# Kernel tuning notes

Measured on AMD Instinct MI355X. Metric: run time of the kernel, lower is better.

The kernel has to match this reference:

```python
import jax, jax.numpy as jnp
import numpy as np

PRE_NMS_THRESH = 0.05
PRE_NMS_TOP_N = 1000
NMS_THRESH = 0.6
FPN_POST_NMS_TOP_N = 100
MIN_SIZE = 0.0
STRIDE = 8
NEG = -1e9  # padding score for invalid slots (avoids inf/nan in grads)


def setup_inputs() -> dict:
    key = jax.random.key(0)
    k1, k2, k3 = jax.random.split(key, 3)
    N, H, W = 16, 400, 608
    # stride-8 FCOS location grid, xy order
    xs = (jnp.arange(W, dtype=jnp.float32) * STRIDE) + STRIDE // 2
    ys = (jnp.arange(H, dtype=jnp.float32) * STRIDE) + STRIDE // 2
    gy, gx = jnp.meshgrid(ys, xs, indexing='ij')
    locations = jnp.stack([gx.reshape(-1), gy.reshape(-1)], axis=1)  # [H*W, 2]
    box_cls = jax.random.normal(k1, (N, 1, H, W), dtype=jnp.float32)
    box_regression = jax.random.uniform(k2, (N, 4, H, W), dtype=jnp.float32) * 64.0
    centerness = jax.random.normal(k3, (N, 1, H, W), dtype=jnp.float32)
    image_sizes = jnp.tile(jnp.array([[H * STRIDE, W * STRIDE]], dtype=jnp.int32), (N, 1))  # (h, w)
    return {"locations": locations, "box_cls": box_cls,
            "box_regression": box_regression, "centerness": centerness,
            "image_sizes": image_sizes}


def _nms_one(boxes, scores):
    """Greedy NMS over K fixed slots. boxes [K,4], scores [K] (NEG = invalid)."""
    order = jnp.argsort(-scores)
    b = boxes[order]
    s = scores[order]
    area = (b[:, 2] - b[:, 0]) * (b[:, 3] - b[:, 1])
    lt = jnp.maximum(b[:, None, :2], b[None, :, :2])   # [K,K,2]
    rb = jnp.minimum(b[:, None, 2:], b[None, :, 2:])
    wh = jnp.clip(rb - lt, 0.0)
    inter = wh[..., 0] * wh[..., 1]
    iou = inter / (area[:, None] + area[None, :] - inter + 1e-9)
    K = b.shape[0]
    ar = jnp.arange(K)

    def body(keep, i):
        kept_i = keep[i] & (s[i] > NEG / 2)
        keep = keep & ~(kept_i & (iou[i] > NMS_THRESH) & (ar > i))
        return keep, kept_i

    _, kept = jax.lax.scan(body, jnp.ones((K,), dtype=bool), ar)
    s_out = jnp.where(kept & (s > NEG / 2), s, NEG)
    return b, s_out


def reference(locations, box_cls, box_regression, centerness, image_sizes):
    N, C, H, W = box_cls.shape
    # [N,C,H,W] -> [N,H*W,C] ; BINARY, num_classes=2 -> C=1
    scores = jax.nn.sigmoid(box_cls.transpose(0, 2, 3, 1).reshape(N, -1))  # [N,HW]
    reg = box_regression.transpose(0, 2, 3, 1).reshape(N, -1, 4)           # [N,HW,4]
    ctr = jax.nn.sigmoid(centerness.transpose(0, 2, 3, 1).reshape(N, -1))  # [N,HW]
    cand = scores > PRE_NMS_THRESH           # candidate mask from raw cls score
    s = scores * ctr                         # score used for ranking
    sm = jnp.where(cand, s, NEG)
    vals, idx = jax.lax.top_k(sm, PRE_NMS_TOP_N)                 # [N,K]
    valid = jnp.take_along_axis(cand, idx, axis=1)               # [N,K]
    g_reg = jnp.take_along_axis(reg, idx[..., None], axis=1)     # [N,K,4]
    g_loc = locations[idx]                                       # [N,K,2]
    x1 = g_loc[..., 0] - g_reg[..., 0]
    y1 = g_loc[..., 1] - g_reg[..., 1]
    x2 = g_loc[..., 0] + g_reg[..., 2]
    y2 = g_loc[..., 1] + g_reg[..., 3]
    hw = image_sizes.astype(jnp.float32)
    wmax = hw[:, 1:2] - 1.0
    hmax = hw[:, 0:1] - 1.0
    x1 = jnp.clip(x1, 0.0, wmax); x2 = jnp.clip(x2, 0.0, wmax)
    y1 = jnp.clip(y1, 0.0, hmax); y2 = jnp.clip(y2, 0.0, hmax)
    keep_size = ((x2 - x1 + 1.0) >= MIN_SIZE) & ((y2 - y1 + 1.0) >= MIN_SIZE)
    valid = valid & keep_size
    boxes = jnp.stack([x1, y1, x2, y2], axis=-1)                 # [N,K,4]
    sc = jnp.where(valid, vals, NEG)
    b_sorted, s_nms = jax.vmap(_nms_one)(boxes, sc)              # [N,K,4],[N,K]
    fv, fi = jax.lax.top_k(s_nms, FPN_POST_NMS_TOP_N)            # [N,100]
    fb = jnp.take_along_axis(b_sorted, fi[..., None], axis=1)    # [N,100,4]
    fvalid = fv > NEG / 2
    fb = jnp.where(fvalid[..., None], fb, 0.0)
    fs = jnp.where(fvalid, fv, 0.0)
    labels = jnp.where(fvalid, 1, 0).astype(jnp.int32)
    dets = jnp.concatenate([fb, fs[..., None]], axis=-1)         # [N,100,5]
    return dets, labels, fvalid
```

## Files before the change

### kernel.cpp

```cpp
#include <hip/hip_runtime.h>
#include <cstdint>


#define NIMG 16
#define WW 608
#define HW 243200
#define NF4 60800
#define TOPK 1000
#define NBINS 512
#define NB2 2048
#define SCAN_BLOCKS 60
#define SCAN_THREADS 256
#define F4_PER_BLOCK 1024
#define LS 128
#define PCAP 1024
#define MCAP 2048
#define EDS_CAP 512
#define NEGV (-1e9f)

__device__ __forceinline__ float sigm(float x) { return 1.0f / (1.0f + expf(-x)); }

__device__ __forceinline__ int binof(float v) {
  if (!(v > 0.0f)) return 0;
  int b = (int)(v * (float)NBINS);
  return b > (NBINS - 1) ? (NBINS - 1) : b;
}

__device__ __forceinline__ int bucketof(float v) {
  if (!(v > 0.0f)) return 0;
  int b = (int)(v * (float)NB2);
  return b > (NB2 - 1) ? (NB2 - 1) : b;
}

__device__ __forceinline__ void find_thresh_bin(const unsigned* h, const unsigned* chunk,
                                                unsigned T, unsigned* outbs, int tid) {
  unsigned v = (tid < 32) ? chunk[tid] : 0u;
  unsigned inc = v;
#pragma unroll
  for (int d = 1; d < 32; d <<= 1) {
    unsigned o = __shfl_down(inc, d, 64);
    if (tid + d < 32) inc += o;
  }
  unsigned long long m = __ballot((tid < 32) && (inc >= T));
  if (m == 0ull) { if (tid == 0) *outbs = 0u; return; }
  int cc = 63 - __clzll(m);
  unsigned above = __shfl(inc, cc) - chunk[cc];
  unsigned v2 = (tid < 16) ? h[cc * 16 + tid] : 0u;
  unsigned inc2 = v2;
#pragma unroll
  for (int d = 1; d < 16; d <<= 1) {
    unsigned o = __shfl_down(inc2, d, 64);
    if (tid + d < 16) inc2 += o;
  }
  unsigned long long m2 = __ballot((tid < 16) && (above + inc2 >= T));
  int bb = (m2 != 0ull) ? (63 - __clzll(m2)) : 0;
  if (tid == 0) *outbs = (unsigned)(cc * 16 + bb);
}

__global__ __launch_bounds__(SCAN_THREADS) void k_scanstore(
    const float4* __restrict__ cls, const float4* __restrict__ ctr,
    unsigned long long* __restrict__ pre, unsigned* __restrict__ pcnt) {
  __shared__ unsigned lh[NBINS];
  __shared__ unsigned long long plist[PCAP];
  __shared__ unsigned chunk[NBINS / 16];
  __shared__ unsigned sLb, pcl;
  const int tid = threadIdx.x;
  for (int b = tid; b < NBINS; b += SCAN_THREADS) lh[b] = 0u;
  if (tid == 0) pcl = 0u;
  __syncthreads();
  const int n = blockIdx.y;
  const float4* c4 = cls + (size_t)n * NF4;
  const float4* t4 = ctr + (size_t)n * NF4;
  const int base = blockIdx.x * F4_PER_BLOCK;
  float4 cv[4], tv[4];
  float smr[16];
  bool ok[4];
#pragma unroll
  for (int e = 0; e < 4; ++e) {
    int i = base + e * SCAN_THREADS + tid;
    ok[e] = (i < NF4);
    if (ok[e]) { cv[e] = c4[i]; tv[e] = t4[i]; }
  }
#pragma unroll
  for (int e = 0; e < 4; ++e) {
    const float* cc = (const float*)&cv[e];
    const float* tt = (const float*)&tv[e];
#pragma unroll
    for (int k = 0; k < 4; ++k) {
      float sm = NEGV;
      if (ok[e]) {
        float sc = sigm(cc[k]);
        sm = (sc > 0.05f) ? sc * sigm(tt[k]) : NEGV;
        atomicAdd(&lh[binof(sm)], 1u);
      }
      smr[e * 4 + k] = sm;
    }
  }
  __syncthreads();
  if (tid < NBINS / 16) {
    unsigned s = 0;
    for (int k = 0; k < 16; ++k) s += lh[tid * 16 + k];
    chunk[tid] = s;
  }
  __syncthreads();
  if (tid < 64) find_thresh_bin(lh, chunk, LS, &sLb, tid);
  __syncthreads();
  const unsigned Lb = sLb;
#pragma unroll
  for (int e = 0; e < 4; ++e) {
    if (ok[e]) {
#pragma unroll
      for (int k = 0; k < 4; ++k) {
        float sm = smr[e * 4 + k];
        if ((unsigned)binof(sm) >= Lb) {
          unsigned gi = (unsigned)((base + e * SCAN_THREADS + tid) * 4 + k);
          unsigned p = atomicAdd(&pcl, 1u);
          if (p < PCAP)
            plist[p] = ((unsigned long long)__float_as_uint(sm) << 32) |
                       (unsigned long long)(~gi);
        }
      }
    }
  }
  __syncthreads();
  const int bslot = n * SCAN_BLOCKS + blockIdx.x;
  unsigned m = pcl; if (m > PCAP) m = PCAP;
  unsigned long long* gp = pre + (size_t)bslot * PCAP;
  for (unsigned k = tid; k < m; k += SCAN_THREADS) gp[k] = plist[k];
  if (tid == 0) pcnt[bslot] = m;
}

__global__ __launch_bounds__(1024) void k_fcr_nms(
    const unsigned long long* __restrict__ pre, const unsigned* __restrict__ pcnt,
    const float* __restrict__ reg, const int* __restrict__ isz,
    float* __restrict__ out) {
  __shared__ __align__(16) unsigned long long smemA[2816];
  __shared__ __align__(16) unsigned long long smemB[MCAP];
  __shared__ unsigned bh[NB2];
  __shared__ unsigned bbase[NB2];
  __shared__ unsigned chunk[32];
  __shared__ unsigned offs[SCAN_BLOCKS + 1];
  __shared__ unsigned wsum[16];
  __shared__ unsigned sB2, mc, ecl;
  const int n = blockIdx.x;
  const int tid = threadIdx.x;
  const int wid = tid >> 6, lane = tid & 63;
  unsigned long long* sk = smemB;

  for (int b = tid; b < NB2; b += 1024) bh[b] = 0u;
  if (tid < 64) {
    int l = tid;
    int v = (l < SCAN_BLOCKS) ? (int)pcnt[n * SCAN_BLOCKS + l] : 0;
    int inc = v;
#pragma unroll
    for (int d = 1; d < 64; d <<= 1) {
      int o = __shfl_up(inc, d, 64);
      if (l >= d) inc += o;
    }
    if (l < SCAN_BLOCKS) offs[l + 1] = (unsigned)inc;
    if (l == 0) offs[0] = 0u;
  }
  __syncthreads();
  const unsigned P = offs[SCAN_BLOCKS];
  const unsigned long long* pbase = pre + (size_t)n * SCAN_BLOCKS * PCAP;
  for (unsigned p = tid; p < P; p += 1024) {
    int lo = 0, hi = SCAN_BLOCKS - 1;
    while (lo < hi) {
      int mid = (lo + hi + 1) >> 1;
      if (offs[mid] <= p) lo = mid; else hi = mid - 1;
    }
    unsigned long long key = pbase[(size_t)lo * PCAP + (p - offs[lo])];
    float v = __uint_as_float((unsigned)(key >> 32));
    atomicAdd(&bh[bucketof(v)], 1u);
  }
  __syncthreads();
  if (tid < 32) {
    unsigned s = 0;
    const int b0 = tid * 64;
    for (int k = 0; k < 64; ++k) s += bh[b0 + k];
    chunk[tid] = s;
  }
  __syncthreads();
  if (tid < 64) {
    unsigned v = (tid < 32) ? chunk[tid] : 0u;
    unsigned inc = v;
#pragma unroll
    for (int d = 1; d < 32; d <<= 1) {
      unsigned o = __shfl_down(inc, d, 64);
      if (tid + d < 32) inc += o;
    }
    unsigned long long m = __ballot((tid < 32) && (inc >= TOPK));
    int cc = (m != 0ull) ? (63 - __clzll(m)) : 0;
    unsigned above = (m != 0ull) ? (__shfl(inc, cc) - chunk[cc]) : 0u;
    unsigned inc2 = bh[cc * 64 + tid];
#pragma unroll
    for (int d = 1; d < 64; d <<= 1) {
      unsigned o = __shfl_down(inc2, d, 64);
      if (tid + d < 64) inc2 += o;
    }
    unsigned long long m2 = __ballot(above + inc2 >= TOPK);
    int bb = (m2 != 0ull) ? (63 - __clzll(m2)) : 0;
    if (tid == 0) sB2 = (m != 0ull) ? (unsigned)(cc * 64 + bb) : 0u;
  }
  __syncthreads();
  const unsigned B2 = sB2;
  {
    int g0 = tid * 2, g1 = g0 + 1;
    unsigned a0 = bh[NB2 - 1 - g0];
    unsigned a1 = bh[NB2 - 1 - g1];
    unsigned pair = a0 + a1;
    unsigned inc = pair;
#pragma unroll
    for (int d = 1; d < 64; d <<= 1) {
      unsigned o = __shfl_up(inc, d, 64);
      if (lane >= d) inc += o;
    }
    if (lane == 63) wsum[wid] = inc;
    __syncthreads();
    if (tid < 64) {
      unsigned v = (tid < 16) ? wsum[tid] : 0u;
      unsigned i2 = v;
#pragma unroll
      for (int d = 1; d < 16; d <<= 1) {
        unsigned o = __shfl_up(i2, d, 64);
        if (tid >= d) i2 += o;
      }
      if (tid < 16) wsum[tid] = i2 - v;
    }
    __syncthreads();
    unsigned excl = inc - pair + wsum[wid];
    bbase[NB2 - 1 - g0] = excl;
    bbase[NB2 - 1 - g1] = excl + a0;
  }
  __syncthreads();
  if (tid == 0) {
    unsigned mm = bbase[B2] + bh[B2];
    mc = (mm > MCAP) ? MCAP : mm;
  }
  for (int b = tid; b < NB2; b += 1024) bh[b] = 0u;
  __syncthreads();
  const unsigned M = mc;
  for (unsigned p = tid; p < P; p += 1024) {
    int lo = 0, hi = SCAN_BLOCKS - 1;
    while (lo < hi) {
      int mid = (lo + hi + 1) >> 1;
      if (offs[mid] <= p) lo = mid; else hi = mid - 1;
    }
    unsigned long long key = pbase[(size_t)lo * PCAP + (p - offs[lo])];
    float v = __uint_as_float((unsigned)(key >> 32));
    int b = bucketof(v);
    if ((unsigned)b >= B2) {
      unsigned pos = bbase[b] + atomicAdd(&bh[b], 1u);
      if (pos < MCAP) sk[pos] = key;
    }
  }
  float4* sb = (float4*)smemA;
  float* ssc = (float*)((char*)smemA + 16384);
  unsigned char* kept = (unsigned char*)((char*)smemA + 20480);
  int* sel = (int*)((char*)smemA + 21600);
  if (tid < TOPK) { sb[tid] = make_float4(0.f, 0.f, 0.f, 0.f); ssc[tid] = NEGV; }
  __syncthreads();
  const float wmax = (float)(isz[n * 2 + 1] - 1);
  const float hmax = (float)(isz[n * 2 + 0] - 1);
  const float* rg = reg + (size_t)n * 4 * HW;
  for (unsigned s = tid; s < M; s += 1024) {
    const unsigned long long mykey = sk[s];
    int b = bucketof(__uint_as_float((unsigned)(mykey >> 32)));
    unsigned beg = bbase[b];
    unsigned end = (b > 0) ? bbase[b - 1] : M;
    if (end > M) end = M;
    unsigned rank = beg;
    for (unsigned t = beg; t < end; ++t) rank += (sk[t] > mykey) ? 1u : 0u;
    if (rank >= TOPK) continue;
    const unsigned gi = ~(unsigned)(mykey & 0xFFFFFFFFull);
    const float val = __uint_as_float((unsigned)(mykey >> 32));
    int wx = (int)gi % WW, hy = (int)gi / WW;
    float lx = (float)(wx * 8 + 4), ly = (float)(hy * 8 + 4);
    float l = rg[0 * HW + gi], tt = rg[1 * HW + gi];
    float rr = rg[2 * HW + gi], bb2 = rg[3 * HW + gi];
    float x1 = lx - l, y1 = ly - tt, x2 = lx + rr, y2 = ly + bb2;
    x1 = fminf(fmaxf(x1, 0.0f), wmax);
    x2 = fminf(fmaxf(x2, 0.0f), wmax);
    y1 = fminf(fmaxf(y1, 0.0f), hmax);
    y2 = fminf(fmaxf(y2, 0.0f), hmax);
    float scr = val;
    if (!(((x2 - x1 + 1.0f) >= 0.0f) && ((y2 - y1 + 1.0f) >= 0.0f))) {
      scr = NEGV; x1 = y1 = x2 = y2 = 0.0f;
    }
    sb[rank] = make_float4(x1, y1, x2, y2);
    ssc[rank] = scr;
  }
  __syncthreads();
  unsigned* ccount = bh;
  unsigned* cidx = bh + 1024;
  unsigned* cbase = bbase;
  unsigned* eds = bbase + 1024;
  unsigned* eds2 = bbase + 1536;
  const int W = isz[n * 2 + 1], H = isz[n * 2 + 0];
  int cw = (W + 31) >> 5; if (cw < 128) cw = 128;
  int ch = (H + 31) >> 5; if (ch < 128) ch = 128;
  const int cols = (W + cw - 1) / cw;
  const int rows = (H + ch - 1) / ch;
  const float icw = 1.0f / (float)cw, ich = 1.0f / (float)ch;
  ccount[tid & 1023] = 0u;
  if (tid == 0) ecl = 0u;
  __syncthreads();
  int mycell = -1;
  if (tid < TOPK && ssc[tid] > NEGV * 0.5f) {
    float4 b = sb[tid];
    int cx = (int)((b.x + b.z) * 0.5f * icw);
    int cy = (int)((b.y + b.w) * 0.5f * ich);
    cx = cx < 0 ? 0 : (cx > cols - 1 ? cols - 1 : cx);
    cy = cy < 0 ? 0 : (cy > rows - 1 ? rows - 1 : cy);
    mycell = cy * cols + cx;
    atomicAdd(&ccount[mycell], 1u);
  }
  __syncthreads();
  {
    unsigned v = ccount[tid];
    unsigned inc = v;
#pragma unroll
    for (int d = 1; d < 64; d <<= 1) {
      unsigned o = __shfl_up(inc, d, 64);
      if (lane >= d) inc += o;
    }
    if (lane == 63) wsum[wid] = inc;
    __syncthreads();
    if (tid < 64) {
      unsigned vv = (tid < 16) ? wsum[tid] : 0u;
      unsigned i2 = vv;
#pragma unroll
      for (int d = 1; d < 16; d <<= 1) {
        unsigned o = __shfl_up(i2, d, 64);
        if (tid >= d) i2 += o;
      }
      if (tid < 16) wsum[tid] = i2 - vv;
    }
    __syncthreads();
    cbase[tid] = inc - v + wsum[wid];
  }
  __syncthreads();
  ccount[tid] = 0u;
  __syncthreads();
  if (mycell >= 0) {
    unsigned pos = cbase[mycell] + atomicAdd(&ccount[mycell], 1u);
    cidx[pos] = (unsigned)tid;
  }
  __syncthreads();
  if (mycell >= 0) {
    const int j = tid;
    float4 bj = sb[j];
    float aj = (bj.z - bj.x) * (bj.w - bj.y);
    int cx = mycell % cols, cy = mycell / cols;
    int x0 = cx > 0 ? cx - 1 : 0, x1c = cx < cols - 1 ? cx + 1 : cols - 1;
    int y0 = cy > 0 ? cy - 1 : 0, y1c = cy < rows - 1 ? cy + 1 : rows - 1;
    for (int yy = y0; yy <= y1c; ++yy) {
      for (int xx = x0; xx <= x1c; ++xx) {
        unsigned c = (unsigned)(yy * cols + xx);
        unsigned b0 = cbase[c], cnt = ccount[c];
        for (unsigned k2 = 0; k2 < cnt; ++k2) {
          unsigned i = cidx[b0 + k2];
          if (i >= (unsigned)j) continue;
          float4 bi = sb[i];
          float ai = (bi.z - bi.x) * (bi.w - bi.y);
          float ltx = fmaxf(bi.x, bj.x), lty = fmaxf(bi.y, bj.y);
          float rbx = fminf(bi.z, bj.z), rby = fminf(bi.w, bj.w);
          float wv = fmaxf(rbx - ltx, 0.0f), hv = fmaxf(rby - lty, 0.0f);
          float inter = wv * hv;
          float iou = inter / (ai + aj - inter + 1e-9f);
          if (iou > 0.6f) {
            unsigned p2 = atomicAdd(&ecl, 1u);
            if (p2 < EDS_CAP) eds[p2] = (i << 10) | (unsigned)j;
          }
        }
      }
    }
  }
  __syncthreads();
  unsigned E = ecl; if (E > EDS_CAP) E = EDS_CAP;
  for (int k = tid; k < TOPK; k += 1024) kept[k] = 1;
  __syncthreads();
  for (int e = tid; e < (int)E; e += 1024) {
    unsigned v = eds[e];
    unsigned r = 0;
    for (unsigned t = 0; t < E; ++t) r += (eds[t] < v) ? 1u : 0u;
    eds2[r] = v;
  }
  __syncthreads();
  if (tid == 0) {
    for (int e = 0; e < (int)E; ++e) {
      unsigned i2 = eds2[e] >> 10, j2 = eds2[e] & 1023u;
      if (kept[i2]) kept[j2] = 0;
    }
  }
  __syncthreads();
  if (tid < 100) sel[tid] = -1;
  __syncthreads();
  if (tid < 64) {
    int c0 = tid * 16;
    int c1 = c0 + 16; if (c1 > TOPK) c1 = TOPK;
    int cnt = 0;
    for (int e = c0; e < c1; ++e)
      if (kept[e] && ssc[e] > NEGV * 0.5f) cnt++;
    int inc = cnt;
#pragma unroll
    for (int d = 1; d < 64; d <<= 1) {
      int o = __shfl_up(inc, d, 64);
      if (tid >= d) inc += o;
    }
    unsigned r = (unsigned)(inc - cnt);
    for (int e = c0; e < c1; ++e) {
      if (kept[e] && ssc[e] > NEGV * 0.5f) {
        if (r < 100u) sel[r] = e;
        r++;
      }
    }
  }
  __syncthreads();
  for (int k = tid; k < 100; k += 1024) {
    int s = sel[k];
    float x1 = 0.f, y1 = 0.f, x2 = 0.f, y2 = 0.f, sc = 0.f, lab = 0.f, fv = 0.f;
    if (s >= 0) {
      float4 b = sb[s];
      x1 = b.x; y1 = b.y; x2 = b.z; y2 = b.w;
      sc = ssc[s]; lab = 1.0f; fv = 1.0f;
    }
    int o = (n * 100 + k) * 5;
    out[o + 0] = x1; out[o + 1] = y1; out[o + 2] = x2; out[o + 3] = y2; out[o + 4] = sc;
    out[NIMG * 500 + n * 100 + k] = lab;
    out[NIMG * 600 + n * 100 + k] = fv;
  }
}

extern "C" void kernel_launch(void* const* d_in, const int* in_sizes, int n_in,
                              void* d_out, int out_size, void* d_ws, size_t ws_size,
                              hipStream_t stream) {
  const float4* cls4 = (const float4*)d_in[1];
  const float* reg = (const float*)d_in[2];
  const float4* ctr4 = (const float4*)d_in[3];
  const int* isz = (const int*)d_in[4];
  float* out = (float*)d_out;
  uint8_t* w = (uint8_t*)d_ws;

  uint8_t* p = w;
  unsigned long long* pre = (unsigned long long*)p; p += (size_t)NIMG * SCAN_BLOCKS * PCAP * 8;
  unsigned* pcnt = (unsigned*)p;   p += (size_t)NIMG * SCAN_BLOCKS * 4;
  (void)ws_size;

  dim3 g1(SCAN_BLOCKS, NIMG);
  k_scanstore<<<g1, SCAN_THREADS, 0, stream>>>(cls4, ctr4, pre, pcnt);
  k_fcr_nms<<<NIMG, 1024, 0, stream>>>(pre, pcnt, reg, isz, out);
}
```

Before: 56.71 us.

## Decode candidate boxes in scan kernel instead of serial NMS block

Box decoding, which gathers the regression values and clips them, moves from the single-block-per-image NMS kernel into the widely parallel scan kernel. Each candidate's box is written to a structure-of-arrays workspace, and the NMS kernel copies it into shared memory during bucket scatter. This takes the scattered global gathers off the critical path of the 16-block kernel. In exchange the scan kernel decodes every pre-candidate, more than the final top 1000, and the NMS kernel uses more shared memory (an extra 32KB box array), which could hurt occupancy or exceed limits.

```diff
diff --git a/kernel.cpp b/kernel.cpp
--- a/kernel.cpp
+++ b/kernel.cpp
@@ -59,9 +59,12 @@
 
 __global__ __launch_bounds__(SCAN_THREADS) void k_scanstore(
     const float4* __restrict__ cls, const float4* __restrict__ ctr,
-    unsigned long long* __restrict__ pre, unsigned* __restrict__ pcnt) {
+    const float* __restrict__ reg, const int* __restrict__ isz,
+    float* __restrict__ preval, unsigned* __restrict__ pregi,
+    float4* __restrict__ prebox, unsigned* __restrict__ pcnt) {
   __shared__ unsigned lh[NBINS];
-  __shared__ unsigned long long plist[PCAP];
+  __shared__ float lval[PCAP];
+  __shared__ unsigned lgi[PCAP];
   __shared__ unsigned chunk[NBINS / 16];
   __shared__ unsigned sLb, pcl;
   const int tid = threadIdx.x;
@@ -115,9 +118,7 @@
         if ((unsigned)binof(sm) >= Lb) {
           unsigned gi = (unsigned)((base + e * SCAN_THREADS + tid) * 4 + k);
           unsigned p = atomicAdd(&pcl, 1u);
-          if (p < PCAP)
-            plist[p] = ((unsigned long long)__float_as_uint(sm) << 32) |
-                       (unsigned long long)(~gi);
+          if (p < PCAP) { lval[p] = sm; lgi[p] = gi; }
         }
       }
     }
@@ -125,17 +126,39 @@
   __syncthreads();
   const int bslot = n * SCAN_BLOCKS + blockIdx.x;
   unsigned m = pcl; if (m > PCAP) m = PCAP;
-  unsigned long long* gp = pre + (size_t)bslot * PCAP;
-  for (unsigned k = tid; k < m; k += SCAN_THREADS) gp[k] = plist[k];
+  const float wmax = (float)(isz[n * 2 + 1] - 1);
+  const float hmax = (float)(isz[n * 2 + 0] - 1);
+  const float* rg = reg + (size_t)n * 4 * HW;
+  const size_t gbase = (size_t)bslot * PCAP;
+  for (unsigned k = tid; k < m; k += SCAN_THREADS) {
+    unsigned gi = lgi[k];
+    float val = lval[k];
+    int wx = (int)gi % WW, hy = (int)gi / WW;
+    float lx = (float)(wx * 8 + 4), ly = (float)(hy * 8 + 4);
+    float l = rg[0 * HW + gi], tt = rg[1 * HW + gi];
+    float rr = rg[2 * HW + gi], bb = rg[3 * HW + gi];
+    float x1 = lx - l, y1 = ly - tt, x2 = lx + rr, y2 = ly + bb;
+    x1 = fminf(fmaxf(x1, 0.0f), wmax);
+    x2 = fminf(fmaxf(x2, 0.0f), wmax);
+    y1 = fminf(fmaxf(y1, 0.0f), hmax);
+    y2 = fminf(fmaxf(y2, 0.0f), hmax);
+    bool valid = (((x2 - x1 + 1.0f) >= 0.0f) && ((y2 - y1 + 1.0f) >= 0.0f));
+    float4 bx = valid ? make_float4(x1, y1, x2, y2)
+                      : make_float4(-1.f, -1.f, -1.f, -1.f);
+    preval[gbase + k] = val;
+    pregi[gbase + k] = gi;
+    prebox[gbase + k] = bx;
+  }
   if (tid == 0) pcnt[bslot] = m;
 }
 
 __global__ __launch_bounds__(1024) void k_fcr_nms(
-    const unsigned long long* __restrict__ pre, const unsigned* __restrict__ pcnt,
-    const float* __restrict__ reg, const int* __restrict__ isz,
-    float* __restrict__ out) {
+    const float* __restrict__ preval, const unsigned* __restrict__ pregi,
+    const float4* __restrict__ prebox, const unsigned* __restrict__ pcnt,
+    const int* __restrict__ isz, float* __restrict__ out) {
   __shared__ __align__(16) unsigned long long smemA[2816];
-  __shared__ __align__(16) unsigned long long smemB[MCAP];
+  __shared__ __align__(16) unsigned long long sk[MCAP];
+  __shared__ __align__(16) float4 skbox[MCAP];
   __shared__ unsigned bh[NB2];
   __shared__ unsigned bbase[NB2];
   __shared__ unsigned chunk[32];
@@ -145,7 +168,6 @@
   const int n = blockIdx.x;
   const int tid = threadIdx.x;
   const int wid = tid >> 6, lane = tid & 63;
-  unsigned long long* sk = smemB;
 
   for (int b = tid; b < NB2; b += 1024) bh[b] = 0u;
   if (tid < 64) {
@@ -162,15 +184,14 @@
   }
   __syncthreads();
   const unsigned P = offs[SCAN_BLOCKS];
-  const unsigned long long* pbase = pre + (size_t)n * SCAN_BLOCKS * PCAP;
+  const size_t ibase = (size_t)n * SCAN_BLOCKS * PCAP;
   for (unsigned p = tid; p < P; p += 1024) {
     int lo = 0, hi = SCAN_BLOCKS - 1;
     while (lo < hi) {
       int mid = (lo + hi + 1) >> 1;
       if (offs[mid] <= p) lo = mid; else hi = mid - 1;
     }
-    unsigned long long key = pbase[(size_t)lo * PCAP + (p - offs[lo])];
-    float v = __uint_as_float((unsigned)(key >> 32));
+    float v = preval[ibase + (size_t)lo * PCAP + (p - offs[lo])];
     atomicAdd(&bh[bucketof(v)], 1u);
   }
   __syncthreads();
@@ -246,12 +267,17 @@
       int mid = (lo + hi + 1) >> 1;
       if (offs[mid] <= p) lo = mid; else hi = mid - 1;
     }
-    unsigned long long key = pbase[(size_t)lo * PCAP + (p - offs[lo])];
-    float v = __uint_as_float((unsigned)(key >> 32));
+    size_t idx = ibase + (size_t)lo * PCAP + (p - offs[lo]);
+    float v = preval[idx];
     int b = bucketof(v);
     if ((unsigned)b >= B2) {
+      unsigned gi = pregi[idx];
       unsigned pos = bbase[b] + atomicAdd(&bh[b], 1u);
-      if (pos < MCAP) sk[pos] = key;
+      if (pos < MCAP) {
+        sk[pos] = ((unsigned long long)__float_as_uint(v) << 32) |
+                  (unsigned long long)(~gi);
+        skbox[pos] = prebox[idx];
+      }
     }
   }
   float4* sb = (float4*)smemA;
@@ -260,35 +286,19 @@
   int* sel = (int*)((char*)smemA + 21600);
   if (tid < TOPK) { sb[tid] = make_float4(0.f, 0.f, 0.f, 0.f); ssc[tid] = NEGV; }
   __syncthreads();
-  const float wmax = (float)(isz[n * 2 + 1] - 1);
-  const float hmax = (float)(isz[n * 2 + 0] - 1);
-  const float* rg = reg + (size_t)n * 4 * HW;
   for (unsigned s = tid; s < M; s += 1024) {
     const unsigned long long mykey = sk[s];
-    int b = bucketof(__uint_as_float((unsigned)(mykey >> 32)));
+    const float val = __uint_as_float((unsigned)(mykey >> 32));
+    int b = bucketof(val);
     unsigned beg = bbase[b];
     unsigned end = (b > 0) ? bbase[b - 1] : M;
     if (end > M) end = M;
     unsigned rank = beg;
     for (unsigned t = beg; t < end; ++t) rank += (sk[t] > mykey) ? 1u : 0u;
     if (rank >= TOPK) continue;
-    const unsigned gi = ~(unsigned)(mykey & 0xFFFFFFFFull);
-    const float val = __uint_as_float((unsigned)(mykey >> 32));
-    int wx = (int)gi % WW, hy = (int)gi / WW;
-    float lx = (float)(wx * 8 + 4), ly = (float)(hy * 8 + 4);
-    float l = rg[0 * HW + gi], tt = rg[1 * HW + gi];
-    float rr = rg[2 * HW + gi], bb2 = rg[3 * HW + gi];
-    float x1 = lx - l, y1 = ly - tt, x2 = lx + rr, y2 = ly + bb2;
-    x1 = fminf(fmaxf(x1, 0.0f), wmax);
-    x2 = fminf(fmaxf(x2, 0.0f), wmax);
-    y1 = fminf(fmaxf(y1, 0.0f), hmax);
-    y2 = fminf(fmaxf(y2, 0.0f), hmax);
-    float scr = val;
-    if (!(((x2 - x1 + 1.0f) >= 0.0f) && ((y2 - y1 + 1.0f) >= 0.0f))) {
-      scr = NEGV; x1 = y1 = x2 = y2 = 0.0f;
-    }
-    sb[rank] = make_float4(x1, y1, x2, y2);
-    ssc[rank] = scr;
+    float4 bx = skbox[s];
+    sb[rank] = bx;
+    ssc[rank] = (bx.x < 0.0f) ? NEGV : val;
   }
   __syncthreads();
   unsigned* ccount = bh;
@@ -302,7 +312,7 @@
   const int cols = (W + cw - 1) / cw;
   const int rows = (H + ch - 1) / ch;
   const float icw = 1.0f / (float)cw, ich = 1.0f / (float)ch;
-  ccount[tid & 1023] = 0u;
+  ccount[tid] = 0u;
   if (tid == 0) ecl = 0u;
   __syncthreads();
   int mycell = -1;
@@ -442,12 +452,16 @@
   float* out = (float*)d_out;
   uint8_t* w = (uint8_t*)d_ws;
 
+  const size_t NSLOT = (size_t)NIMG * SCAN_BLOCKS * PCAP;
   uint8_t* p = w;
-  unsigned long long* pre = (unsigned long long*)p; p += (size_t)NIMG * SCAN_BLOCKS * PCAP * 8;
-  unsigned* pcnt = (unsigned*)p;   p += (size_t)NIMG * SCAN_BLOCKS * 4;
+  float* preval = (float*)p;      p += NSLOT * 4;
+  unsigned* pregi = (unsigned*)p; p += NSLOT * 4;
+  float4* prebox = (float4*)p;    p += NSLOT * 16;
+  unsigned* pcnt = (unsigned*)p;  p += (size_t)NIMG * SCAN_BLOCKS * 4;
   (void)ws_size;
 
   dim3 g1(SCAN_BLOCKS, NIMG);
-  k_scanstore<<<g1, SCAN_THREADS, 0, stream>>>(cls4, ctr4, pre, pcnt);
-  k_fcr_nms<<<NIMG, 1024, 0, stream>>>(pre, pcnt, reg, isz, out);
-}
+  k_scanstore<<<g1, SCAN_THREADS, 0, stream>>>(cls4, ctr4, reg, isz,
+                                               preval, pregi, prebox, pcnt);
+  k_fcr_nms<<<NIMG, 1024, 0, stream>>>(preval, pregi, prebox, pcnt, isz, out);
+}
```

New measurement: 56.78 us. No clear change (+0.1%).
